# Performance work log

Hardware: AMD Instinct MI355X
Metric: run time of the kernel (lower is better)

Reference implementation:

```python
import jax, jax.numpy as jnp
import numpy as np

B, S, F, D = 2, 576, 16, 512   # batch, spatial tokens (24x24), frames, query_dim
H, C = 8, 64                   # heads, dim_head; inner = H*C = 512


def setup_inputs() -> dict:
    key = jax.random.key(0)
    ks = jax.random.split(key, 6)
    x = jax.random.normal(ks[0], (B, S, F, D), jnp.float32)
    # alternating drop pattern over frames 2..F-1; identical per batch row,
    # as the module requires (it reshapes kept indices to [bs, -1] and takes
    # valid_num from row 0)
    pat = jnp.tile(jnp.array([1, 0], jnp.int64), (F - 2) // 2)
    drop_mask = jnp.broadcast_to(pat, (B, F - 2))
    sd = 1.0 / np.sqrt(D)
    Wq = jax.random.normal(ks[1], (D, H * C), jnp.float32) * sd
    Wk = jax.random.normal(ks[2], (D, H * C), jnp.float32) * sd
    Wv = jax.random.normal(ks[3], (D, H * C), jnp.float32) * sd
    Wout = jax.random.normal(ks[4], (H * C, D), jnp.float32) * (1.0 / np.sqrt(H * C))
    bout = jnp.zeros((D,), jnp.float32)
    return {"x": x, "drop_mask": drop_mask, "Wq": Wq, "Wk": Wk, "Wv": Wv,
            "Wout": Wout, "bout": bout}


def _sdpa(q, k, v):
    # q: [..., Lq, C], k/v: [..., Lk, C]; xformers default scale = 1/sqrt(C)
    scale = 1.0 / np.sqrt(q.shape[-1])
    logits = jnp.einsum('...qc,...kc->...qk', q, k) * scale
    w = jax.nn.softmax(logits, axis=-1)
    return jnp.einsum('...qk,...kc->...qc', w, v)


def reference(x, drop_mask, Wq, Wk, Wv, Wout, bout):
    b, s, f, _ = x.shape
    h, c = H, C
    q = x @ Wq  # [b, s, f, h*c]
    k = x @ Wk
    v = x @ Wv

    # ---- per-frame spatial self-attention for frames 1: ('b s f (h c) -> (b f h) s c')
    def to_bfhsc(t, nf):
        return t.reshape(b, s, nf, h, c).transpose(0, 2, 3, 1, 4)  # b f h s c

    ress = _sdpa(to_bfhsc(q[:, :, 1:], f - 1),
                 to_bfhsc(k[:, :, 1:], f - 1),
                 to_bfhsc(v[:, :, 1:], f - 1))            # [b, f-1, h, s, c]
    ress = ress.transpose(0, 3, 1, 2, 4).reshape(b, s, f - 1, h * c)

    # ---- frame-0 temporal attention over first 2 frames + non-dropped frames
    dm = np.asarray(drop_mask)
    valid = int((f - 2) - dm[0].sum())
    # kept frame indices (into frames 2..f-1), per batch row
    kept = np.stack([np.nonzero(dm[i] == 0)[0] for i in range(b)])  # [b, valid]
    idx = jnp.asarray(kept)[:, None, :, None]
    ka, va = k[:, :, 2:], v[:, :, 2:]                     # [b, s, f-2, h*c]
    ki = jnp.take_along_axis(ka, jnp.broadcast_to(idx, (b, s, valid, h * c)), axis=2)
    vi = jnp.take_along_axis(va, jnp.broadcast_to(idx, (b, s, valid, h * c)), axis=2)
    dk = jnp.concatenate([k[:, :, :2], ki], axis=2)        # [b, s, df, h*c]
    dv = jnp.concatenate([v[:, :, :2], vi], axis=2)
    df = 2 + valid

    qt = q[:, :, 0].reshape(b, s, h, c).transpose(0, 2, 1, 3)  # [b, h, s, c]
    kt = dk.reshape(b, s, df, h, c).transpose(0, 3, 1, 2, 4).reshape(b, h, s * df, c)
    vt = dv.reshape(b, s, df, h, c).transpose(0, 3, 1, 2, 4).reshape(b, h, s * df, c)
    resq = _sdpa(qt, kt, vt)                               # [b, h, s, c]
    resq = resq.transpose(0, 2, 1, 3).reshape(b, s, 1, h * c)

    res = jnp.concatenate([resq, ress], axis=2)            # [b, s, f, h*c]
    return res @ Wout + bout                               # [b, s, f, D]
```

## Files before the change

kernel.cpp:

```cpp
#include <hip/hip_runtime.h>
#include <math.h>

#define Bb 2
#define Ss 576
#define Ff 16
#define Hh 8
#define Cc 64
#define HC 512
#define Mrows (Bb * Ss * Ff)

typedef __bf16 bf16x8 __attribute__((ext_vector_type(8)));
typedef float  f32x4  __attribute__((ext_vector_type(4)));
typedef float  f32x16 __attribute__((ext_vector_type(16)));
typedef unsigned short u16;
typedef unsigned int   u32;

#if __has_builtin(__builtin_amdgcn_exp2f)
#define EXP2(x) __builtin_amdgcn_exp2f(x)
#else
#define EXP2(x) exp2f(x)
#endif

#define QSCALE 0.18033688011112042f

__device__ __forceinline__ u16 f2bf(float f) {
    union { __bf16 b; u16 u; } cv;
    cv.b = (__bf16)f;
    return cv.u;
}

__device__ __forceinline__ f32x16 zero16() {
    f32x16 z;
#pragma unroll
    for (int i = 0; i < 16; ++i) z[i] = 0.f;
    return z;
}

__device__ __forceinline__ int swz8(int row, int g) {
    return row * 64 + (((g ^ (row & 7) ^ (((row >> 3) & 1) << 1)) & 7) << 3);
}
__device__ __forceinline__ int swzg(int row, int g) {
    return row * 32 + (((g ^ (row & 3)) & 3) << 3);
}

__device__ __forceinline__ uint4 pack8(float4 a, float4 b) {
    union { u16 s[8]; uint4 v; } u;
    u.s[0] = f2bf(a.x); u.s[1] = f2bf(a.y); u.s[2] = f2bf(a.z); u.s[3] = f2bf(a.w);
    u.s[4] = f2bf(b.x); u.s[5] = f2bf(b.y); u.s[6] = f2bf(b.z); u.s[7] = f2bf(b.w);
    return u.v;
}

__global__ __launch_bounds__(256) void convert_w_kernel(
    const float* __restrict__ W0, const float* __restrict__ W1,
    const float* __restrict__ W2, const float* __restrict__ W3,
    u16* __restrict__ Wt)
{
    __shared__ float Ts[64][65];
    const int mz = blockIdx.z;
    const float* W = (mz == 0) ? W0 : (mz == 1) ? W1 : (mz == 2) ? W2 : W3;
    u16* Wo = Wt + (size_t)mz * 512 * 512;
    const int k0 = blockIdx.x * 64, n0 = blockIdx.y * 64;
    const int t = threadIdx.x;
#pragma unroll
    for (int p = 0; p < 4; ++p) {
        int idx = t + p * 256;
        int row = idx >> 4, cg = idx & 15;
        *(float4*)&Ts[row][cg * 4] =
            *(const float4*)&W[(size_t)(k0 + row) * 512 + n0 + cg * 4];
    }
    __syncthreads();
#pragma unroll
    for (int p = 0; p < 2; ++p) {
        int idx = t + p * 256;
        int row = idx >> 3, cg = idx & 7;
        union { u16 s[8]; uint4 v; } u;
#pragma unroll
        for (int j = 0; j < 8; ++j) u.s[j] = f2bf(Ts[cg * 8 + j][row]);
        *(uint4*)&Wo[(size_t)(n0 + row) * 512 + k0 + cg * 8] = u.v;
    }
}

__global__ __launch_bounds__(256) void qkv_kernel(
    const float* __restrict__ x, const u16* __restrict__ Wt,
    u16* __restrict__ q, u16* __restrict__ k, u16* __restrict__ vT)
{
    __shared__ u16 As[128 * 32];
    __shared__ u16 Bs[128 * 32];
    const int bi = blockIdx.x;
    const int mt = bi % 144;
    const int mm = bi / 144;
    const int nt = mm & 3, mat = mm >> 2;
    const int t = threadIdx.x;
    const int w = t >> 6, L = t & 63;
    const int m0 = mt * 128, n0 = nt * 128;
    const int wm = (w >> 1) * 64, wn = (w & 1) * 64;

    const int srow = t >> 2, scg = t & 3;
    const int ma0 = m0 + srow, ma1 = m0 + srow + 64;
    const int b0 = ma0 / 9216, r0 = ma0 % 9216, f0 = r0 / 576, s0 = r0 % 576;
    const int b1 = ma1 / 9216, r1 = ma1 % 9216, f1 = r1 / 576, s1 = r1 % 576;
    const float* xp0 = x + ((size_t)(b0 * 576 + s0) * 16 + f0) * 512 + scg * 8;
    const float* xp1 = x + ((size_t)(b1 * 576 + s1) * 16 + f1) * 512 + scg * 8;
    const u16* Bp = Wt + (size_t)mat * 512 * 512 + (size_t)(n0 + srow) * 512 + scg * 8;
    const int lo0 = swzg(srow, scg), lo1 = swzg(srow + 64, scg);

    float4 fa0 = *(const float4*)xp0, fa0b = *(const float4*)(xp0 + 4);
    float4 fa1 = *(const float4*)xp1, fa1b = *(const float4*)(xp1 + 4);
    uint4 ub0 = *(const uint4*)Bp;
    uint4 ub1 = *(const uint4*)(Bp + 64 * 512);

    f32x4 acc[4][4];
#pragma unroll
    for (int i = 0; i < 4; ++i)
#pragma unroll
        for (int j = 0; j < 4; ++j) acc[i][j] = (f32x4){0.f, 0.f, 0.f, 0.f};

    for (int k0 = 0; k0 < 512; k0 += 32) {
        __syncthreads();
        *(uint4*)&As[lo0] = pack8(fa0, fa0b);
        *(uint4*)&As[lo1] = pack8(fa1, fa1b);
        *(uint4*)&Bs[lo0] = ub0;
        *(uint4*)&Bs[lo1] = ub1;
        __syncthreads();
        if (k0 < 480) {
            fa0  = *(const float4*)(xp0 + k0 + 32);
            fa0b = *(const float4*)(xp0 + k0 + 36);
            fa1  = *(const float4*)(xp1 + k0 + 32);
            fa1b = *(const float4*)(xp1 + k0 + 36);
            ub0  = *(const uint4*)(Bp + k0 + 32);
            ub1  = *(const uint4*)(Bp + k0 + 32 + 64 * 512);
        }
        bf16x8 af[4], bfr[4];
#pragma unroll
        for (int i = 0; i < 4; ++i) {
            af[i]  = *(const bf16x8*)&As[swzg(wm + 16 * i + (L & 15), L >> 4)];
            bfr[i] = *(const bf16x8*)&Bs[swzg(wn + 16 * i + (L & 15), L >> 4)];
        }
#pragma unroll
        for (int i = 0; i < 4; ++i)
#pragma unroll
            for (int j = 0; j < 4; ++j)
                acc[i][j] = __builtin_amdgcn_mfma_f32_16x16x32_bf16(
                    af[i], bfr[j], acc[i][j], 0, 0, 0);
    }

    if (mat < 2) {
        u16* Cout = (mat == 0) ? q : k;
        const float scale = (mat == 0) ? QSCALE : 1.0f;
#pragma unroll
        for (int i = 0; i < 4; ++i)
#pragma unroll
            for (int j = 0; j < 4; ++j)
#pragma unroll
                for (int r = 0; r < 4; ++r) {
                    int row = m0 + wm + 16 * i + (L >> 4) * 4 + r;
                    int col = n0 + wn + 16 * j + (L & 15);
                    float vv = acc[i][j][r] * scale;
                    float pvv = __shfl_xor(vv, 1);
                    if (!(L & 1)) {
                        u32 pk2 = (u32)f2bf(vv) | ((u32)f2bf(pvv) << 16);
                        *(u32*)(Cout + (size_t)row * 512 + col) = pk2;
                    }
                }
    } else {
#pragma unroll
        for (int i = 0; i < 4; ++i) {
            int row = m0 + wm + 16 * i + (L >> 4) * 4;
            int bb = row / 9216, rr = row % 9216;
            int f = rr / 576, s = rr % 576;
#pragma unroll
            for (int j = 0; j < 4; ++j) {
                int col = n0 + wn + 16 * j + (L & 15);
                int h = col >> 6, c = col & 63;
                union { u16 s4[4]; uint2 v; } u;
#pragma unroll
                for (int r = 0; r < 4; ++r) u.s4[r] = f2bf(acc[i][j][r]);
                *(uint2*)&vT[((((size_t)(bb * 16 + f) * 8 + h) * 64 + c) * 576) + s] = u.v;
            }
        }
    }
}

__global__ __launch_bounds__(256) void gemm_out_kernel(
    const u16* __restrict__ res, const u16* __restrict__ Wt3,
    const float* __restrict__ bout, float* __restrict__ out)
{
    __shared__ u16 As[128 * 32];
    __shared__ u16 Bs[128 * 32];
    const int bi = blockIdx.x;
    const int mt = bi % 144, nt = bi / 144;
    const int t = threadIdx.x;
    const int w = t >> 6, L = t & 63;
    const int m0 = mt * 128, n0 = nt * 128;
    const int wm = (w >> 1) * 64, wn = (w & 1) * 64;

    const int srow = t >> 2, scg = t & 3;
    const u16* Ap = res + (size_t)(m0 + srow) * 512 + scg * 8;
    const u16* Bp = Wt3 + (size_t)(n0 + srow) * 512 + scg * 8;
    const int lo0 = swzg(srow, scg), lo1 = swzg(srow + 64, scg);

    uint4 ua0 = *(const uint4*)Ap;
    uint4 ua1 = *(const uint4*)(Ap + 64 * 512);
    uint4 ub0 = *(const uint4*)Bp;
    uint4 ub1 = *(const uint4*)(Bp + 64 * 512);

    f32x4 acc[4][4];
#pragma unroll
    for (int i = 0; i < 4; ++i)
#pragma unroll
        for (int j = 0; j < 4; ++j) acc[i][j] = (f32x4){0.f, 0.f, 0.f, 0.f};

    for (int k0 = 0; k0 < 512; k0 += 32) {
        __syncthreads();
        *(uint4*)&As[lo0] = ua0;
        *(uint4*)&As[lo1] = ua1;
        *(uint4*)&Bs[lo0] = ub0;
        *(uint4*)&Bs[lo1] = ub1;
        __syncthreads();
        if (k0 < 480) {
            ua0 = *(const uint4*)(Ap + k0 + 32);
            ua1 = *(const uint4*)(Ap + k0 + 32 + 64 * 512);
            ub0 = *(const uint4*)(Bp + k0 + 32);
            ub1 = *(const uint4*)(Bp + k0 + 32 + 64 * 512);
        }
        bf16x8 af[4], bfr[4];
#pragma unroll
        for (int i = 0; i < 4; ++i) {
            af[i]  = *(const bf16x8*)&As[swzg(wm + 16 * i + (L & 15), L >> 4)];
            bfr[i] = *(const bf16x8*)&Bs[swzg(wn + 16 * i + (L & 15), L >> 4)];
        }
#pragma unroll
        for (int i = 0; i < 4; ++i)
#pragma unroll
            for (int j = 0; j < 4; ++j)
                acc[i][j] = __builtin_amdgcn_mfma_f32_16x16x32_bf16(
                    af[i], bfr[j], acc[i][j], 0, 0, 0);
    }

#pragma unroll
    for (int i = 0; i < 4; ++i)
#pragma unroll
        for (int r = 0; r < 4; ++r) {
            int row = m0 + wm + 16 * i + (L >> 4) * 4 + r;
            int bb = row / 9216, rr = row % 9216;
            int f = rr / 576, s = rr % 576;
            size_t obase = ((size_t)(bb * 576 + s) * 16 + f) * 512;
#pragma unroll
            for (int j = 0; j < 4; ++j) {
                int col = n0 + wn + 16 * j + (L & 15);
                out[obase + col] = acc[i][j][r] + bout[col];
            }
        }
}

__global__ __launch_bounds__(256, 4) void attn_kernel(
    const u16* __restrict__ q, const u16* __restrict__ k,
    const u16* __restrict__ vT, const int* __restrict__ dm,
    u16* __restrict__ res, float* __restrict__ po, float* __restrict__ pl)
{
    __shared__ u16 Ks[64 * 64];
    __shared__ u16 Vts[64 * 64];

    const int t = threadIdx.x;
    const int w = t >> 6, L = t & 63;
    const int half = L >> 5, l31 = L & 31;
    const int bi = blockIdx.x;

    int b, h, qt, qframe, fi, mode;
    if (bi < 720) {
        mode = 0;
        qt = bi / 144;
        int g = bi % 144;
        int bh = g / 9; fi = g % 9;
        b = bh >> 3; h = bh & 7; qframe = 0;
    } else {
        mode = 1;
        int u = bi - 720;
        int g = u % 240;
        qt = u / 240;
        b = g / 120;
        int rr = g % 120;
        qframe = 1 + (rr >> 3); h = rr & 7; fi = 0;
    }

    int kf;
    if (mode == 1) {
        kf = qframe;
    } else if (fi < 2) {
        kf = fi;
    } else {
        int n = 2; kf = 2;
#pragma unroll
        for (int j = 0; j < Ff - 2; ++j) {
            if (dm[b * (Ff - 2) + j] == 0) { if (n == fi) kf = 2 + j; ++n; }
        }
    }

    const int q0 = qt * 128;
    const bool active = (q0 + 32 * w) < Ss;
    const int qrow = q0 + 32 * w + l31;

    bf16x8 qf[4];
    if (active) {
        const u16* qp = q + ((size_t)(b * 16 + qframe) * Ss + qrow) * 512 + h * 64 + 8 * half;
#pragma unroll
        for (int ks = 0; ks < 4; ++ks) qf[ks] = *(const bf16x8*)(qp + 16 * ks);
    }

    float lsum = 0.f;
    f32x16 o[2] = {zero16(), zero16()};

    const int srow = t >> 2, sc2 = (t & 3) * 2;
    const int lk0 = swz8(srow, sc2), lk1 = swz8(srow, sc2 + 1);
    const u16* kbase = k + ((size_t)(b * 16 + kf) * Ss) * 512 + h * 64;
    const u16* vbase = vT + (((size_t)(b * 16 + kf) * 8 + h) * 64) * (size_t)Ss;

    uint4 ka, kb2, va, vb2;
    {
        const u16* kp = kbase + (size_t)srow * 512 + sc2 * 8;
        ka  = *(const uint4*)kp;
        kb2 = *(const uint4*)(kp + 8);
        const u16* vp = vbase + (size_t)srow * Ss + sc2 * 8;
        va  = *(const uint4*)vp;
        vb2 = *(const uint4*)(vp + 8);
    }

    for (int kt = 0; kt < 9; ++kt) {
        __syncthreads();
        *(uint4*)&Ks[lk0]  = ka;
        *(uint4*)&Ks[lk1]  = kb2;
        *(uint4*)&Vts[lk0] = va;
        *(uint4*)&Vts[lk1] = vb2;
        __syncthreads();

        if (kt < 8) {
            int s0 = (kt + 1) * 64;
            const u16* kp = kbase + (size_t)(s0 + srow) * 512 + sc2 * 8;
            ka  = *(const uint4*)kp;
            kb2 = *(const uint4*)(kp + 8);
            const u16* vp = vbase + (size_t)srow * Ss + s0 + sc2 * 8;
            va  = *(const uint4*)vp;
            vb2 = *(const uint4*)(vp + 8);
        }

        if (active) {
#pragma unroll
            for (int hb = 0; hb < 2; ++hb) {
                f32x16 st = zero16();
#pragma unroll
                for (int ks = 0; ks < 4; ++ks) {
                    bf16x8 a = *(const bf16x8*)&Ks[swz8(32 * hb + l31, 2 * ks + half)];
                    st = __builtin_amdgcn_mfma_f32_32x32x16_bf16(a, qf[ks], st, 0, 0, 0);
                }
#pragma unroll
                for (int kk = 0; kk < 2; ++kk) {
                    const int ks = 2 * hb + kk;
                    float e0 = EXP2(st[8 * kk + 0]), e1 = EXP2(st[8 * kk + 1]);
                    float e2 = EXP2(st[8 * kk + 2]), e3 = EXP2(st[8 * kk + 3]);
                    float e4 = EXP2(st[8 * kk + 4]), e5 = EXP2(st[8 * kk + 5]);
                    float e6 = EXP2(st[8 * kk + 6]), e7 = EXP2(st[8 * kk + 7]);
                    lsum += ((e0 + e1) + (e2 + e3)) + ((e4 + e5) + (e6 + e7));
                    u32 x0 = (u32)f2bf(e0) | ((u32)f2bf(e1) << 16);
                    u32 z0 = (u32)f2bf(e2) | ((u32)f2bf(e3) << 16);
                    u32 x1 = (u32)f2bf(e4) | ((u32)f2bf(e5) << 16);
                    u32 z1 = (u32)f2bf(e6) | ((u32)f2bf(e7) << 16);
                    auto sx = __builtin_amdgcn_permlane32_swap(x0, x1, false, false);
                    auto sz = __builtin_amdgcn_permlane32_swap(z0, z1, false, false);
                    union { u32 u[4]; bf16x8 v; } pu;
                    pu.u[0] = sx[0]; pu.u[1] = sz[0]; pu.u[2] = sx[1]; pu.u[3] = sz[1];
                    bf16x8 v0 = *(const bf16x8*)&Vts[swz8(l31,      2 * ks + half)];
                    bf16x8 v1 = *(const bf16x8*)&Vts[swz8(32 + l31, 2 * ks + half)];
                    o[0] = __builtin_amdgcn_mfma_f32_32x32x16_bf16(v0, pu.v, o[0], 0, 0, 0);
                    o[1] = __builtin_amdgcn_mfma_f32_32x32x16_bf16(v1, pu.v, o[1], 0, 0, 0);
                }
            }
        }
    }

    if (!active) return;
    lsum += __shfl_xor(lsum, 32);

    if (mode == 1) {
        float inv = 1.f / lsum;
        u16* rp = res + ((size_t)(b * 16 + qframe) * Ss + qrow) * 512 + h * 64;
#pragma unroll
        for (int cg = 0; cg < 2; ++cg)
#pragma unroll
            for (int g = 0; g < 4; ++g) {
                union { u16 s4[4]; uint2 v; } u;
#pragma unroll
                for (int r = 0; r < 4; ++r) u.s4[r] = f2bf(o[cg][4 * g + r] * inv);
                *(uint2*)&rp[32 * cg + 8 * g + 4 * half] = u.v;
            }
    } else {
        int bh = b * 8 + h;
        float* pp = po + ((size_t)(fi * 16 + bh) * Ss + qrow) * 64;
#pragma unroll
        for (int cg = 0; cg < 2; ++cg)
#pragma unroll
            for (int g = 0; g < 4; ++g) {
                float4 v4 = make_float4(o[cg][4 * g + 0], o[cg][4 * g + 1],
                                        o[cg][4 * g + 2], o[cg][4 * g + 3]);
                *(float4*)&pp[32 * cg + 8 * g + 4 * half] = v4;
            }
        if (half == 0) pl[(size_t)(fi * 16 + bh) * Ss + qrow] = lsum;
    }
}

__global__ __launch_bounds__(256) void merge_kernel(
    const float* __restrict__ po, const float* __restrict__ pl,
    u16* __restrict__ res)
{
    int tid = blockIdx.x * 256 + threadIdx.x;
    int c4 = tid & 15;
    int rem = tid >> 4;
    int qg = rem % Ss;
    int bh = rem / Ss;
    int b = bh >> 3, h = bh & 7;
    float4 acc = make_float4(0.f, 0.f, 0.f, 0.f);
    float ls = 0.f;
#pragma unroll
    for (int fi = 0; fi < 9; ++fi) {
        const float4 v = *(const float4*)&po[((size_t)(fi * 16 + bh) * Ss + qg) * 64 + c4 * 4];
        acc.x += v.x; acc.y += v.y; acc.z += v.z; acc.w += v.w;
        ls += pl[(size_t)(fi * 16 + bh) * Ss + qg];
    }
    float inv = 1.f / ls;
    union { u16 s4[4]; uint2 v; } u;
    u.s4[0] = f2bf(acc.x * inv); u.s4[1] = f2bf(acc.y * inv);
    u.s4[2] = f2bf(acc.z * inv); u.s4[3] = f2bf(acc.w * inv);
    *(uint2*)&res[((size_t)(b * 16 + 0) * Ss + qg) * 512 + h * 64 + c4 * 4] = u.v;
}

extern "C" void kernel_launch(void* const* d_in, const int* in_sizes, int n_in,
                              void* d_out, int out_size, void* d_ws, size_t ws_size,
                              hipStream_t stream)
{
    (void)in_sizes; (void)n_in; (void)out_size; (void)ws_size;
    const float* x    = (const float*)d_in[0];
    const int*   dmsk = (const int*)  d_in[1];
    const float* Wq   = (const float*)d_in[2];
    const float* Wk   = (const float*)d_in[3];
    const float* Wv   = (const float*)d_in[4];
    const float* Wout = (const float*)d_in[5];
    const float* bout = (const float*)d_in[6];
    float* out = (float*)d_out;

    const size_t NE = (size_t)Mrows * HC;
    u16* q   = (u16*)d_ws;
    u16* kk  = q   + NE;
    u16* vT  = kk  + NE;
    u16* res = vT  + NE;
    u16* Wt  = res + NE;
    float* po = (float*)(Wt + (size_t)4 * 512 * 512);
    float* pl = po + (size_t)9 * 16 * Ss * 64;

    convert_w_kernel<<<dim3(8, 8, 4), 256, 0, stream>>>(Wq, Wk, Wv, Wout, Wt);
    qkv_kernel<<<1728, 256, 0, stream>>>(x, Wt, q, kk, vT);
    attn_kernel<<<1920, 256, 0, stream>>>(q, kk, vT, dmsk, res, po, pl);
    merge_kernel<<<576, 256, 0, stream>>>(po, pl, res);
    gemm_out_kernel<<<576, 256, 0, stream>>>(
        res, Wt + (size_t)3 * 512 * 512, bout, out);
}
```

Before: 229.7 us.

## Pre-convert x to bf16 and stage GEMM tiles via direct global-to-LDS loads

Adds a separate kernel that converts x to bf16 into the res workspace buffer, so the QKV GEMM reads half the bytes per pass and no longer packs floats in its inner loop. Both GEMMs now use global_load_lds to copy tiles straight into shared memory, dropping the register staging. This also drops the swizzled LDS layout and the software prefetch of the next k-tile. The risks are LDS bank conflicts on the unswizzled reads, loads no longer overlapping the MFMA work, and an extra full pass over x.

```diff
diff --git a/kernel.cpp b/kernel.cpp
--- a/kernel.cpp
+++ b/kernel.cpp
@@ -39,15 +39,27 @@
 __device__ __forceinline__ int swz8(int row, int g) {
     return row * 64 + (((g ^ (row & 7) ^ (((row >> 3) & 1) << 1)) & 7) << 3);
 }
-__device__ __forceinline__ int swzg(int row, int g) {
-    return row * 32 + (((g ^ (row & 3)) & 3) << 3);
-}
 
 __device__ __forceinline__ uint4 pack8(float4 a, float4 b) {
     union { u16 s[8]; uint4 v; } u;
     u.s[0] = f2bf(a.x); u.s[1] = f2bf(a.y); u.s[2] = f2bf(a.z); u.s[3] = f2bf(a.w);
     u.s[4] = f2bf(b.x); u.s[5] = f2bf(b.y); u.s[6] = f2bf(b.z); u.s[7] = f2bf(b.w);
     return u.v;
+}
+
+__device__ __forceinline__ void gl_lds16(const u16* g, u16* l) {
+    __builtin_amdgcn_global_load_lds(
+        (const __attribute__((address_space(1))) u32*)g,
+        (__attribute__((address_space(3))) u32*)l, 16, 0, 0);
+}
+
+__global__ __launch_bounds__(256) void convert_x_kernel(
+    const float* __restrict__ x, u16* __restrict__ xb)
+{
+    size_t i = ((size_t)blockIdx.x * 256 + threadIdx.x) * 8;
+    float4 a = *(const float4*)&x[i];
+    float4 b = *(const float4*)&x[i + 4];
+    *(uint4*)&xb[i] = pack8(a, b);
 }
 
 __global__ __launch_bounds__(256) void convert_w_kernel(
@@ -81,7 +93,7 @@
 }
 
 __global__ __launch_bounds__(256) void qkv_kernel(
-    const float* __restrict__ x, const u16* __restrict__ Wt,
+    const u16* __restrict__ xb, const u16* __restrict__ Wt,
     u16* __restrict__ q, u16* __restrict__ k, u16* __restrict__ vT)
 {
     __shared__ u16 As[128 * 32];
@@ -96,18 +108,12 @@
     const int wm = (w >> 1) * 64, wn = (w & 1) * 64;
 
     const int srow = t >> 2, scg = t & 3;
-    const int ma0 = m0 + srow, ma1 = m0 + srow + 64;
+    const int ma0 = m0 + srow, ma1 = ma0 + 64;
     const int b0 = ma0 / 9216, r0 = ma0 % 9216, f0 = r0 / 576, s0 = r0 % 576;
     const int b1 = ma1 / 9216, r1 = ma1 % 9216, f1 = r1 / 576, s1 = r1 % 576;
-    const float* xp0 = x + ((size_t)(b0 * 576 + s0) * 16 + f0) * 512 + scg * 8;
-    const float* xp1 = x + ((size_t)(b1 * 576 + s1) * 16 + f1) * 512 + scg * 8;
+    const u16* xp0 = xb + ((size_t)(b0 * 576 + s0) * 16 + f0) * 512 + scg * 8;
+    const u16* xp1 = xb + ((size_t)(b1 * 576 + s1) * 16 + f1) * 512 + scg * 8;
     const u16* Bp = Wt + (size_t)mat * 512 * 512 + (size_t)(n0 + srow) * 512 + scg * 8;
-    const int lo0 = swzg(srow, scg), lo1 = swzg(srow + 64, scg);
-
-    float4 fa0 = *(const float4*)xp0, fa0b = *(const float4*)(xp0 + 4);
-    float4 fa1 = *(const float4*)xp1, fa1b = *(const float4*)(xp1 + 4);
-    uint4 ub0 = *(const uint4*)Bp;
-    uint4 ub1 = *(const uint4*)(Bp + 64 * 512);
 
     f32x4 acc[4][4];
 #pragma unroll
@@ -117,24 +123,16 @@
 
     for (int k0 = 0; k0 < 512; k0 += 32) {
         __syncthreads();
-        *(uint4*)&As[lo0] = pack8(fa0, fa0b);
-        *(uint4*)&As[lo1] = pack8(fa1, fa1b);
-        *(uint4*)&Bs[lo0] = ub0;
-        *(uint4*)&Bs[lo1] = ub1;
-        __syncthreads();
-        if (k0 < 480) {
-            fa0  = *(const float4*)(xp0 + k0 + 32);
-            fa0b = *(const float4*)(xp0 + k0 + 36);
-            fa1  = *(const float4*)(xp1 + k0 + 32);
-            fa1b = *(const float4*)(xp1 + k0 + 36);
-            ub0  = *(const uint4*)(Bp + k0 + 32);
-            ub1  = *(const uint4*)(Bp + k0 + 32 + 64 * 512);
-        }
+        gl_lds16(xp0 + k0, &As[t * 8]);
+        gl_lds16(xp1 + k0, &As[2048 + t * 8]);
+        gl_lds16(Bp + k0, &Bs[t * 8]);
+        gl_lds16(Bp + k0 + 64 * 512, &Bs[2048 + t * 8]);
+        __syncthreads();
         bf16x8 af[4], bfr[4];
 #pragma unroll
         for (int i = 0; i < 4; ++i) {
-            af[i]  = *(const bf16x8*)&As[swzg(wm + 16 * i + (L & 15), L >> 4)];
-            bfr[i] = *(const bf16x8*)&Bs[swzg(wn + 16 * i + (L & 15), L >> 4)];
+            af[i]  = *(const bf16x8*)&As[(wm + 16 * i + (L & 15)) * 32 + (L >> 4) * 8];
+            bfr[i] = *(const bf16x8*)&Bs[(wn + 16 * i + (L & 15)) * 32 + (L >> 4) * 8];
         }
 #pragma unroll
         for (int i = 0; i < 4; ++i)
@@ -197,12 +195,6 @@
     const int srow = t >> 2, scg = t & 3;
     const u16* Ap = res + (size_t)(m0 + srow) * 512 + scg * 8;
     const u16* Bp = Wt3 + (size_t)(n0 + srow) * 512 + scg * 8;
-    const int lo0 = swzg(srow, scg), lo1 = swzg(srow + 64, scg);
-
-    uint4 ua0 = *(const uint4*)Ap;
-    uint4 ua1 = *(const uint4*)(Ap + 64 * 512);
-    uint4 ub0 = *(const uint4*)Bp;
-    uint4 ub1 = *(const uint4*)(Bp + 64 * 512);
 
     f32x4 acc[4][4];
 #pragma unroll
@@ -212,22 +204,16 @@
 
     for (int k0 = 0; k0 < 512; k0 += 32) {
         __syncthreads();
-        *(uint4*)&As[lo0] = ua0;
-        *(uint4*)&As[lo1] = ua1;
-        *(uint4*)&Bs[lo0] = ub0;
-        *(uint4*)&Bs[lo1] = ub1;
-        __syncthreads();
-        if (k0 < 480) {
-            ua0 = *(const uint4*)(Ap + k0 + 32);
-            ua1 = *(const uint4*)(Ap + k0 + 32 + 64 * 512);
-            ub0 = *(const uint4*)(Bp + k0 + 32);
-            ub1 = *(const uint4*)(Bp + k0 + 32 + 64 * 512);
-        }
+        gl_lds16(Ap + k0, &As[t * 8]);
+        gl_lds16(Ap + k0 + 64 * 512, &As[2048 + t * 8]);
+        gl_lds16(Bp + k0, &Bs[t * 8]);
+        gl_lds16(Bp + k0 + 64 * 512, &Bs[2048 + t * 8]);
+        __syncthreads();
         bf16x8 af[4], bfr[4];
 #pragma unroll
         for (int i = 0; i < 4; ++i) {
-            af[i]  = *(const bf16x8*)&As[swzg(wm + 16 * i + (L & 15), L >> 4)];
-            bfr[i] = *(const bf16x8*)&Bs[swzg(wn + 16 * i + (L & 15), L >> 4)];
+            af[i]  = *(const bf16x8*)&As[(wm + 16 * i + (L & 15)) * 32 + (L >> 4) * 8];
+            bfr[i] = *(const bf16x8*)&Bs[(wn + 16 * i + (L & 15)) * 32 + (L >> 4) * 8];
         }
 #pragma unroll
         for (int i = 0; i < 4; ++i)
@@ -454,9 +440,11 @@
     u16* Wt  = res + NE;
     float* po = (float*)(Wt + (size_t)4 * 512 * 512);
     float* pl = po + (size_t)9 * 16 * Ss * 64;
-
+    u16* xb = res;
+
+    convert_x_kernel<<<4608, 256, 0, stream>>>(x, xb);
     convert_w_kernel<<<dim3(8, 8, 4), 256, 0, stream>>>(Wq, Wk, Wv, Wout, Wt);
-    qkv_kernel<<<1728, 256, 0, stream>>>(x, Wt, q, kk, vT);
+    qkv_kernel<<<1728, 256, 0, stream>>>(xb, Wt, q, kk, vT);
     attn_kernel<<<1920, 256, 0, stream>>>(q, kk, vT, dmsk, res, po, pl);
     merge_kernel<<<576, 256, 0, stream>>>(po, pl, res);
     gemm_out_kernel<<<576, 256, 0, stream>>>(
```

Result: no change. 228.5 us (-0.5%).
